# Kernel tuning notes

Measured on AMD Instinct MI355X. Metric: run time of the kernel, lower is better.

The kernel has to match this reference:

```python
import jax, jax.numpy as jnp
import numpy as np

H, DM, DX = 4, 64, 64  # num_heads, out_m_dim, out_x_dim
IN_L, IN_M, IN_X = 128, 128, 128
N, E, E2 = 10000, 160000, 320000


def _edge_softmax(scores, dst, num_nodes):
    # scores: [n_edges, H, 1]; softmax over edges sharing the same dst node
    mx = jax.ops.segment_max(scores, dst, num_segments=num_nodes)
    ex = jnp.exp(scores - mx[dst])
    denom = jax.ops.segment_sum(ex, dst, num_segments=num_nodes)
    return ex / denom[dst]


def setup_inputs() -> dict:
    key = jax.random.key(0)
    ks = jax.random.split(key, 24)

    def xn(k, shape):
        fan = sum(shape)
        return jax.random.normal(k, shape, dtype=jnp.float32) * np.sqrt(2.0 / fan)

    inp = {
        'l_feats': jax.random.normal(ks[0], (N, IN_L), dtype=jnp.float32),
        'm_feats': jax.random.normal(ks[1], (E, IN_M), dtype=jnp.float32),
        'x_feats': jax.random.normal(ks[2], (E2, IN_X), dtype=jnp.float32),
        'g_src': jax.random.randint(ks[3], (E,), 0, N, dtype=jnp.int32),
        'g_dst': jax.random.randint(ks[4], (E,), 0, N, dtype=jnp.int32),
        'lg_src': jax.random.randint(ks[5], (E2,), 0, E, dtype=jnp.int32),
        'lg_dst': jax.random.randint(ks[6], (E2,), 0, E, dtype=jnp.int32),
        # line-graph branch params (torch Linear convention: W [out, in])
        'W_lg_node': xn(ks[7], (DM * H, IN_M + IN_X)),
        'b_lg_node': jnp.zeros((DM * H,), dtype=jnp.float32),
        'W_lg_ni': xn(ks[8], (DX * H, IN_M)),
        'W_lg_fij': xn(ks[9], (DX * H, IN_X)),
        'W_lg_nj': xn(ks[10], (DX * H, IN_M)),
        'lg_attn': xn(ks[11], (1, H, DX)),
        'bias_lg': jnp.zeros((H * DX,), dtype=jnp.float32),
        # base-graph branch params
        'W_g_node': xn(ks[12], (DM * H, IN_M + IN_L)),
        'b_g_node': jnp.zeros((DM * H,), dtype=jnp.float32),
        'W_g_ni': xn(ks[13], (DM * H, IN_L)),
        'W_g_fij': xn(ks[14], (DM * H, IN_M)),
        'W_g_nj': xn(ks[15], (DM * H, IN_L)),
        'g_attn': xn(ks[16], (1, H, DM)),
        'bias_g': jnp.zeros((H * DM,), dtype=jnp.float32),
    }
    return inp


def reference(l_feats, m_feats, x_feats,
              W_lg_node, b_lg_node, W_lg_ni, W_lg_fij, W_lg_nj, lg_attn, bias_lg,
              W_g_node, b_g_node, W_g_ni, W_g_fij, W_g_nj, g_attn, bias_g,
              g_src, g_dst, lg_src, lg_dst):
    n_nodes = l_feats.shape[0]      # graph nodes
    n_lnodes = m_feats.shape[0]     # l_graph nodes == graph edges
    lrelu = jax.nn.leaky_relu       # slope 0.01 (torch default)

    # ---- line-graph attention branch ----
    lg_f_ni = m_feats @ W_lg_ni.T                      # [E, H*DX]
    lg_f_nj = m_feats @ W_lg_nj.T
    lg_f_fij = x_feats @ W_lg_fij.T                    # [E2, H*DX]
    lg_f_out = lrelu(lg_f_ni[lg_src] + lg_f_nj[lg_dst] + lg_f_fij + bias_lg)
    xr = lg_f_out.reshape(-1, H, DX)                   # [E2, H, DX]
    lg_e = jnp.sum(xr * lg_attn, axis=-1, keepdims=True)  # [E2, H, 1]
    a_lg = _edge_softmax(lg_e, lg_dst, n_lnodes)       # [E2, H, 1]

    # mean-aggregate l_graph edge feats onto dst nodes (DGL send_and_recv mean)
    cnt = jax.ops.segment_sum(jnp.ones((lg_dst.shape[0],), dtype=x_feats.dtype),
                              lg_dst, num_segments=n_lnodes)
    agg = jax.ops.segment_sum(x_feats, lg_dst, num_segments=n_lnodes)
    agg = agg / jnp.maximum(cnt, 1.0)[:, None]         # [E, IN_X]

    m1 = jnp.concatenate([m_feats, agg], axis=1)       # [E, IN_M+IN_X]
    h1 = (m1 @ W_lg_node.T + b_lg_node).reshape(-1, H, DM)
    msg1 = h1[lg_src] * a_lg                           # u_mul_e
    h1_dst = jax.ops.segment_sum(msg1, lg_dst, num_segments=n_lnodes)
    lg_h_out = jnp.sum(lrelu(h1_dst), axis=1)          # [E, DM]

    # ---- base-graph attention branch ----
    g_f_ni = l_feats @ W_g_ni.T                        # [N, H*DM]
    g_f_nj = l_feats @ W_g_nj.T
    g_f_fij = m_feats @ W_g_fij.T                      # [E, H*DM]
    g_f_out = lrelu(g_f_ni[g_src] + g_f_nj[g_dst] + g_f_fij + bias_g)
    g_f_out = g_f_out.reshape(-1, H, DM)               # [E, H, DM]
    g_e = jnp.sum(g_f_out * g_attn, axis=-1, keepdims=True)  # [E, H, 1]

    node_edge = l_feats[g_src] + l_feats[g_dst]        # [E, IN_L]
    m2 = jnp.concatenate([node_edge, m_feats], axis=1)  # [E, IN_L+IN_M]
    h2 = (m2 @ W_g_node.T + b_g_node).reshape(-1, H, DM)
    a_g = _edge_softmax(g_e, g_dst, n_nodes)           # [E, H, 1] (per graph edge)
    # l_graph.update_all(u_mul_v): msg[e2] = h2[src(e2)] * a_g[dst(e2)]
    msg2 = h2[lg_src] * a_g[lg_dst]
    h2_dst = jax.ops.segment_sum(msg2, lg_dst, num_segments=n_lnodes)
    g_h_out = jnp.sum(lrelu(h2_dst), axis=1)           # [E, DM]

    return g_h_out + lg_h_out                          # [E, DM]
```

## Files before the change

kernel.cpp:

```cpp
#include <hip/hip_runtime.h>
#include <math.h>

#define LRELU(x) ((x) > 0.0f ? (x) : 0.01f * (x))

typedef __attribute__((ext_vector_type(8))) short short8;
typedef __attribute__((ext_vector_type(4))) float f32x4;

__device__ __forceinline__ unsigned fenc(float f) {
    unsigned u = __float_as_uint(f);
    return (u & 0x80000000u) ? ~u : (u | 0x80000000u);
}
__device__ __forceinline__ float fdec(unsigned u) {
    return __uint_as_float((u & 0x80000000u) ? (u & 0x7FFFFFFFu) : ~u);
}
__device__ __forceinline__ unsigned short f2bf(float f) {
    unsigned u = __float_as_uint(f);
    u += 0x7FFFu + ((u >> 16) & 1u);
    return (unsigned short)(u >> 16);
}
__device__ __forceinline__ float bf2f(unsigned short b) {
    return __uint_as_float(((unsigned)b) << 16);
}
__device__ __forceinline__ ushort4 cvt4(float4 v) {
    ushort4 p;
    p.x = f2bf(v.x); p.y = f2bf(v.y); p.z = f2bf(v.z); p.w = f2bf(v.w);
    return p;
}

__global__ __launch_bounds__(256) void f2bf_k(
    const float* __restrict__ in, unsigned short* __restrict__ out, int n)
{
    for (int i = blockIdx.x * 256 + threadIdx.x; i < n; i += gridDim.x * 256)
        out[i] = f2bf(in[i]);
}

__global__ __launch_bounds__(256) void gemm128_mfma(
    const float* __restrict__ A, const unsigned short* __restrict__ Wbf,
    const float* __restrict__ biasf, unsigned short* __restrict__ Cout, int M)
{
    __shared__ __align__(16) unsigned short smem[64 * 264];
    const int row0 = blockIdx.x * 64;
    const int tid = threadIdx.x;
    const int wv = tid >> 6, lane = tid & 63;
    const int ln = lane & 15, quad = lane >> 4;

    float4 va[8];
#pragma unroll
    for (int k = 0; k < 8; ++k) {
        int i = tid + k * 256;
        int r = row0 + (i >> 5);
        va[k] = make_float4(0.f, 0.f, 0.f, 0.f);
        if (r < M) va[k] = *(const float4*)&A[(size_t)r * 128 + (i & 31) * 4];
    }
#pragma unroll
    for (int k = 0; k < 8; ++k) {
        int i = tid + k * 256;
        *(ushort4*)&smem[(i >> 5) * 136 + (i & 31) * 4] = cvt4(va[k]);
    }
    __syncthreads();

    f32x4 acc[16];
#pragma unroll
    for (int t = 0; t < 16; ++t) acc[t] = (f32x4){0.f, 0.f, 0.f, 0.f};

#pragma unroll 1
    for (int ks = 0; ks < 4; ++ks) {
        short8 a = *(const short8*)&smem[(wv * 16 + ln) * 136 + ks * 32 + quad * 8];
#pragma unroll
        for (int t = 0; t < 16; ++t) {
            short8 b = *(const short8*)&Wbf[(size_t)(t * 16 + ln) * 128 + ks * 32 + quad * 8];
            acc[t] = __builtin_amdgcn_mfma_f32_16x16x32_bf16(a, b, acc[t], 0, 0, 0);
        }
    }
    __syncthreads();

#pragma unroll
    for (int t = 0; t < 16; ++t) {
        int col = t * 16 + ln;
        float bb = biasf ? biasf[col] : 0.0f;
#pragma unroll
        for (int rg = 0; rg < 4; ++rg)
            smem[(wv * 16 + quad * 4 + rg) * 264 + col] = f2bf(acc[t][rg] + bb);
    }
    __syncthreads();
#pragma unroll 1
    for (int i = tid; i < 2048; i += 256) {
        int row = i >> 5, c8 = (i & 31) * 8;
        int r = row0 + row;
        if (r < M) *(short8*)&Cout[(size_t)r * 256 + c8] = *(const short8*)&smem[row * 264 + c8];
    }
}

__global__ __launch_bounds__(256) void gemm_score_mfma(
    const float* __restrict__ A, const unsigned short* __restrict__ Wbf,
    const unsigned short* __restrict__ fni, const unsigned short* __restrict__ fnj,
    const float* __restrict__ bias, const float* __restrict__ attn,
    const int* __restrict__ src, const int* __restrict__ dst,
    float* __restrict__ ebuf, unsigned* __restrict__ smax, int M, int domax)
{
    __shared__ __align__(16) unsigned short smem[64 * 264];
    const int row0 = blockIdx.x * 64;
    const int tid = threadIdx.x;
    const int wv = tid >> 6, lane = tid & 63;
    const int ln = lane & 15, quad = lane >> 4;

    const int rbase = row0 + wv * 16;
    int myr = rbase + ln;
    int msrc = 0, mdst = 0;
    if (myr < M) { msrc = src[myr]; mdst = dst[myr]; }

    float4 va[8];
#pragma unroll
    for (int k = 0; k < 8; ++k) {
        int i = tid + k * 256;
        int r = row0 + (i >> 5);
        va[k] = make_float4(0.f, 0.f, 0.f, 0.f);
        if (r < M) va[k] = *(const float4*)&A[(size_t)r * 128 + (i & 31) * 4];
    }
#pragma unroll
    for (int k = 0; k < 8; ++k) {
        int i = tid + k * 256;
        *(ushort4*)&smem[(i >> 5) * 136 + (i & 31) * 4] = cvt4(va[k]);
    }
    __syncthreads();

    f32x4 acc[16];
#pragma unroll
    for (int t = 0; t < 16; ++t) acc[t] = (f32x4){0.f, 0.f, 0.f, 0.f};

#pragma unroll 1
    for (int ks = 0; ks < 4; ++ks) {
        short8 a = *(const short8*)&smem[(wv * 16 + ln) * 136 + ks * 32 + quad * 8];
#pragma unroll
        for (int t = 0; t < 16; ++t) {
            short8 b = *(const short8*)&Wbf[(size_t)(t * 16 + ln) * 128 + ks * 32 + quad * 8];
            acc[t] = __builtin_amdgcn_mfma_f32_16x16x32_bf16(a, b, acc[t], 0, 0, 0);
        }
    }
    __syncthreads();

    const int c4 = lane * 4;
    const float4 bias4 = *(const float4*)&bias[c4];
    const float4 attn4 = *(const float4*)&attn[c4];

    ushort4 pu[16], pv[16];
#pragma unroll
    for (int j = 0; j < 16; ++j) {
        int s_ = __shfl(msrc, j, 16);
        int d_ = __shfl(mdst, j, 16);
        pu[j] = *(const ushort4*)&fni[(size_t)s_ * 256 + c4];
        pv[j] = *(const ushort4*)&fnj[(size_t)d_ * 256 + c4];
    }

#pragma unroll
    for (int t = 0; t < 16; ++t) {
        int col = t * 16 + ln;
#pragma unroll
        for (int rg = 0; rg < 4; ++rg)
            smem[(wv * 16 + quad * 4 + rg) * 264 + col] = f2bf(acc[t][rg]);
    }

#pragma unroll
    for (int i = 0; i < 16; ++i) {
        int rr = wv * 16 + i;
        int r = row0 + rr;
        if (r >= M) continue;
        int dIdx = __shfl(mdst, i, 16);
        ushort4 f4 = *(const ushort4*)&smem[rr * 264 + c4];
        float v0 = bf2f(f4.x) + bf2f(pu[i].x) + bf2f(pv[i].x) + bias4.x;
        float v1 = bf2f(f4.y) + bf2f(pu[i].y) + bf2f(pv[i].y) + bias4.y;
        float v2 = bf2f(f4.z) + bf2f(pu[i].z) + bf2f(pv[i].z) + bias4.z;
        float v3 = bf2f(f4.w) + bf2f(pu[i].w) + bf2f(pv[i].w) + bias4.w;
        float p = LRELU(v0) * attn4.x + LRELU(v1) * attn4.y
                + LRELU(v2) * attn4.z + LRELU(v3) * attn4.w;
        p += __shfl_xor(p, 1, 64);
        p += __shfl_xor(p, 2, 64);
        p += __shfl_xor(p, 4, 64);
        p += __shfl_xor(p, 8, 64);
        if (ln == 0) {
            ebuf[(size_t)r * 4 + quad] = p;
            if (domax) atomicMax(&smax[(size_t)dIdx * 4 + quad], fenc(p));
        }
    }
}

__global__ __launch_bounds__(256) void gemm256_mfma(
    const float* __restrict__ A0, const void* __restrict__ A1v,
    const int* __restrict__ gsrc, const int* __restrict__ gdst,
    const unsigned short* __restrict__ Wbf, const float* __restrict__ biasf,
    unsigned short* __restrict__ Cout, int M, int mode)
{
    __shared__ __align__(16) unsigned short smem[64 * 264];
    const int row0 = blockIdx.x * 64;
    const int tid = threadIdx.x;
    const int wv = tid >> 6, lane = tid & 63;
    const int ln = lane & 15, quad = lane >> 4;

    if (mode == 0) {
        const unsigned short* A1 = (const unsigned short*)A1v;
        float4 va[8];
#pragma unroll
        for (int k = 0; k < 8; ++k) {
            int i = tid + k * 256;
            int r = row0 + (i >> 5);
            va[k] = make_float4(0.f, 0.f, 0.f, 0.f);
            if (r < M) va[k] = *(const float4*)&A0[(size_t)r * 128 + (i & 31) * 4];
        }
        short8 vb[4];
#pragma unroll
        for (int k = 0; k < 4; ++k) {
            int i = tid + k * 256;
            int r = row0 + (i >> 4);
#pragma unroll
            for (int q = 0; q < 8; ++q) vb[k][q] = 0;
            if (r < M) vb[k] = *(const short8*)&A1[(size_t)r * 128 + (i & 15) * 8];
        }
#pragma unroll
        for (int k = 0; k < 8; ++k) {
            int i = tid + k * 256;
            *(ushort4*)&smem[(i >> 5) * 264 + (i & 31) * 4] = cvt4(va[k]);
        }
#pragma unroll
        for (int k = 0; k < 4; ++k) {
            int i = tid + k * 256;
            *(short8*)&smem[(i >> 4) * 264 + 128 + (i & 15) * 8] = vb[k];
        }
    } else {
        const float* A1 = (const float*)A1v;
        int is[8], id[8];
#pragma unroll
        for (int k = 0; k < 8; ++k) {
            int i = tid + k * 256;
            int r = row0 + (i >> 5);
            is[k] = (r < M) ? gsrc[r] : 0;
            id[k] = (r < M) ? gdst[r] : 0;
        }
        float4 va[8], vb2[8], vc[8];
#pragma unroll
        for (int k = 0; k < 8; ++k) {
            int i = tid + k * 256;
            int r = row0 + (i >> 5);
            int c4i = (i & 31) * 4;
            va[k]  = *(const float4*)&A0[(size_t)is[k] * 128 + c4i];
            vb2[k] = *(const float4*)&A0[(size_t)id[k] * 128 + c4i];
            vc[k] = make_float4(0.f, 0.f, 0.f, 0.f);
            if (r < M) vc[k] = *(const float4*)&A1[(size_t)r * 128 + c4i];
        }
#pragma unroll
        for (int k = 0; k < 8; ++k) {
            int i = tid + k * 256;
            int r = row0 + (i >> 5);
            int c4i = (i & 31) * 4;
            float4 v = make_float4(va[k].x + vb2[k].x, va[k].y + vb2[k].y,
                                   va[k].z + vb2[k].z, va[k].w + vb2[k].w);
            if (r >= M) v = make_float4(0.f, 0.f, 0.f, 0.f);
            *(ushort4*)&smem[(i >> 5) * 264 + c4i] = cvt4(v);
            *(ushort4*)&smem[(i >> 5) * 264 + 128 + c4i] = cvt4(vc[k]);
        }
    }
    __syncthreads();

    f32x4 acc[16];
#pragma unroll
    for (int t = 0; t < 16; ++t) acc[t] = (f32x4){0.f, 0.f, 0.f, 0.f};

#pragma unroll 1
    for (int ks = 0; ks < 8; ++ks) {
        short8 a = *(const short8*)&smem[(wv * 16 + ln) * 264 + ks * 32 + quad * 8];
#pragma unroll
        for (int t = 0; t < 16; ++t) {
            short8 b = *(const short8*)&Wbf[(size_t)(t * 16 + ln) * 256 + ks * 32 + quad * 8];
            acc[t] = __builtin_amdgcn_mfma_f32_16x16x32_bf16(a, b, acc[t], 0, 0, 0);
        }
    }
    __syncthreads();

#pragma unroll
    for (int t = 0; t < 16; ++t) {
        int col = t * 16 + ln;
        float bb = biasf[col];
#pragma unroll
        for (int rg = 0; rg < 4; ++rg)
            smem[(wv * 16 + quad * 4 + rg) * 264 + col] = f2bf(acc[t][rg] + bb);
    }
    __syncthreads();
#pragma unroll 1
    for (int i = tid; i < 2048; i += 256) {
        int row = i >> 5, c8 = (i & 31) * 8;
        int r = row0 + row;
        if (r < M) *(short8*)&Cout[(size_t)r * 256 + c8] = *(const short8*)&smem[row * 264 + c8];
    }
}

__global__ __launch_bounds__(256) void edge_exp(
    float* __restrict__ ebuf, const unsigned* __restrict__ smax,
    float* __restrict__ sden, const int* __restrict__ dst, int nE)
{
    int i = blockIdx.x * 256 + threadIdx.x;
    if (i >= nE * 4) return;
    int e = i >> 2, h = i & 3;
    int d = dst[e];
    float m = fdec(smax[(size_t)d * 4 + h]);
    float ex = expf(ebuf[i] - m);
    ebuf[i] = ex;
    atomicAdd(&sden[(size_t)d * 4 + h], ex);
}

__global__ __launch_bounds__(256) void count_k(
    const int* __restrict__ dst, int* __restrict__ cnt, int n)
{
    int i = blockIdx.x * 256 + threadIdx.x;
    if (i < n) atomicAdd(&cnt[dst[i]], 1);
}

__global__ __launch_bounds__(256) void scan1(
    const int* __restrict__ cnt, int* __restrict__ excl, int* __restrict__ bsum, int n)
{
    __shared__ int sd[256];
    int tid = threadIdx.x;
    int i = blockIdx.x * 256 + tid;
    int v = (i < n) ? cnt[i] : 0;
    sd[tid] = v;
    __syncthreads();
    for (int off2 = 1; off2 < 256; off2 <<= 1) {
        int t = (tid >= off2) ? sd[tid - off2] : 0;
        __syncthreads();
        sd[tid] += t;
        __syncthreads();
    }
    if (i < n) excl[i] = sd[tid] - v;
    if (tid == 255) bsum[blockIdx.x] = sd[255];
}

__global__ __launch_bounds__(1024) void scan2(int* __restrict__ bsum, int nb)
{
    __shared__ int sd[1024];
    int tid = threadIdx.x;
    int v = (tid < nb) ? bsum[tid] : 0;
    sd[tid] = v;
    __syncthreads();
    for (int off2 = 1; off2 < 1024; off2 <<= 1) {
        int t = (tid >= off2) ? sd[tid - off2] : 0;
        __syncthreads();
        sd[tid] += t;
        __syncthreads();
    }
    if (tid < nb) bsum[tid] = sd[tid] - v;
}

__global__ __launch_bounds__(256) void scan3(
    int* __restrict__ excl, const int* __restrict__ bsum, int n, int total)
{
    int i = blockIdx.x * 256 + threadIdx.x;
    if (i < n) excl[i] += bsum[i >> 8];
    if (i == 0) excl[n] = total;
}

__global__ __launch_bounds__(256) void fill_k(
    const int* __restrict__ dst, const int* __restrict__ row_ptr,
    int* __restrict__ cursor, int* __restrict__ colidx, int n)
{
    int i = blockIdx.x * 256 + threadIdx.x;
    if (i >= n) return;
    int d = dst[i];
    int p = atomicAdd(&cursor[d], 1);
    colidx[row_ptr[d] + p] = i;
}

__global__ __launch_bounds__(256) void agg_gather(
    const int* __restrict__ row_ptr, const int* __restrict__ colidx,
    const float* __restrict__ x, unsigned short* __restrict__ aggbf, int nE)
{
    const int lane = threadIdx.x & 63;
    const int d = blockIdx.x * 4 + (threadIdx.x >> 6);
    if (d >= nE) return;
    int b = row_ptr[d], en = row_ptr[d + 1];
    float s0 = 0.f, s1 = 0.f;
    for (int k = b; k < en; ++k) {
        int e = colidx[k];
        float2 v = *(const float2*)&x[(size_t)e * 128 + lane * 2];
        s0 += v.x; s1 += v.y;
    }
    float c = fmaxf((float)(en - b), 1.0f);
    ushort2 o;
    o.x = f2bf(s0 / c); o.y = f2bf(s1 / c);
    *(ushort2*)&aggbf[(size_t)d * 128 + lane * 2] = o;
}

__global__ __launch_bounds__(256) void final_agg(
    const int* __restrict__ row_ptr, const int* __restrict__ colidx,
    const int* __restrict__ lg_src, const float* __restrict__ e_lg,
    const unsigned* __restrict__ lgmax,
    const unsigned short* __restrict__ h1, const unsigned short* __restrict__ h2,
    const float* __restrict__ e_g, const float* __restrict__ gden,
    const int* __restrict__ g_dst, float* __restrict__ out, int nE)
{
    const int lane = threadIdx.x & 63;
    const int d = blockIdx.x * 4 + (threadIdx.x >> 6);
    if (d >= nE) return;
    int b = row_ptr[d], en = row_ptr[d + 1];

    uint4 mu = *(const uint4*)&lgmax[(size_t)d * 4];
    float mx0 = fdec(mu.x), mx1 = fdec(mu.y), mx2 = fdec(mu.z), mx3 = fdec(mu.w);

    float den0 = 0.f, den1 = 0.f, den2 = 0.f, den3 = 0.f;
    float a10 = 0.f, a11 = 0.f, a12 = 0.f, a13 = 0.f;
    float a20 = 0.f, a21 = 0.f, a22 = 0.f, a23 = 0.f;
    for (int k = b; k < en; ++k) {
        int e = colidx[k];
        float4 sc = *(const float4*)&e_lg[(size_t)e * 4];
        float w0 = expf(sc.x - mx0), w1 = expf(sc.y - mx1);
        float w2 = expf(sc.z - mx2), w3 = expf(sc.w - mx3);
        den0 += w0; den1 += w1; den2 += w2; den3 += w3;
        int s = lg_src[e];
        const unsigned short* p1 = &h1[(size_t)s * 256 + lane];
        const unsigned short* p2 = &h2[(size_t)s * 256 + lane];
        a10 += bf2f(p1[0])   * w0;
        a11 += bf2f(p1[64])  * w1;
        a12 += bf2f(p1[128]) * w2;
        a13 += bf2f(p1[192]) * w3;
        a20 += bf2f(p2[0]);
        a21 += bf2f(p2[64]);
        a22 += bf2f(p2[128]);
        a23 += bf2f(p2[192]);
    }
    float o = 0.f;
    if (en > b) {
        float v0 = a10 / den0, v1 = a11 / den1, v2 = a12 / den2, v3 = a13 / den3;
        o += LRELU(v0) + LRELU(v1) + LRELU(v2) + LRELU(v3);
    }
    int gd = g_dst[d];
    float g0 = e_g[(size_t)d * 4 + 0] / gden[(size_t)gd * 4 + 0] * a20;
    float g1 = e_g[(size_t)d * 4 + 1] / gden[(size_t)gd * 4 + 1] * a21;
    float g2 = e_g[(size_t)d * 4 + 2] / gden[(size_t)gd * 4 + 2] * a22;
    float g3 = e_g[(size_t)d * 4 + 3] / gden[(size_t)gd * 4 + 3] * a23;
    o += LRELU(g0) + LRELU(g1) + LRELU(g2) + LRELU(g3);
    out[(size_t)d * 64 + lane] = o;
}

extern "C" void kernel_launch(void* const* d_in, const int* in_sizes, int n_in,
                              void* d_out, int out_size, void* d_ws, size_t ws_size,
                              hipStream_t stream)
{
    const float* l_feats   = (const float*)d_in[0];
    const float* m_feats   = (const float*)d_in[1];
    const float* x_feats   = (const float*)d_in[2];
    const int*   g_src     = (const int*)d_in[3];
    const int*   g_dst     = (const int*)d_in[4];
    const int*   lg_src    = (const int*)d_in[5];
    const int*   lg_dst    = (const int*)d_in[6];
    const float* W_lg_node = (const float*)d_in[7];
    const float* b_lg_node = (const float*)d_in[8];
    const float* W_lg_ni   = (const float*)d_in[9];
    const float* W_lg_fij  = (const float*)d_in[10];
    const float* W_lg_nj   = (const float*)d_in[11];
    const float* lg_attn   = (const float*)d_in[12];
    const float* bias_lg   = (const float*)d_in[13];
    const float* W_g_node  = (const float*)d_in[14];
    const float* b_g_node  = (const float*)d_in[15];
    const float* W_g_ni    = (const float*)d_in[16];
    const float* W_g_fij   = (const float*)d_in[17];
    const float* W_g_nj    = (const float*)d_in[18];
    const float* g_attn    = (const float*)d_in[19];
    const float* bias_g    = (const float*)d_in[20];

    const int N  = in_sizes[0] / 128;
    const int E  = in_sizes[3];
    const int E2 = in_sizes[5];

    float* ws = (float*)d_ws;
    size_t off = 0;
    auto alloc = [&](size_t n) { float* p = ws + off; off += n; return p; };

    unsigned short* wbuf = (unsigned short*)alloc(163840);
    unsigned short* wgni_bf    = wbuf;
    unsigned short* wgnj_bf    = wbuf + 32768;
    unsigned short* wlgni_bf   = wbuf + 65536;
    unsigned short* wlgnj_bf   = wbuf + 98304;
    unsigned short* wlgfij_bf  = wbuf + 131072;
    unsigned short* wgfij_bf   = wbuf + 163840;
    unsigned short* wlgnode_bf = wbuf + 196608;
    unsigned short* wgnode_bf  = wbuf + 262144;

    unsigned short* ni_lg = (unsigned short*)alloc((size_t)E * 128);
    unsigned short* nj_lg = (unsigned short*)alloc((size_t)E * 128);
    unsigned short* gni   = (unsigned short*)alloc((size_t)N * 128);
    unsigned short* gnj   = (unsigned short*)alloc((size_t)N * 128);
    unsigned short* aggbf = (unsigned short*)alloc((size_t)E * 64);
    float* e_lg  = alloc((size_t)E2 * 4);
    float* e_g   = alloc((size_t)E * 4);
    unsigned* gmax = (unsigned*)alloc((size_t)N * 4);
    float* gden  = alloc((size_t)N * 4);
    unsigned* lgmax = (unsigned*)alloc((size_t)E * 4);
    int* row_ptr = (int*)alloc((size_t)E + 4);
    int* colidx  = (int*)alloc((size_t)E2);
    int* cnt     = (int*)alloc((size_t)E);
    int* cursor  = (int*)alloc((size_t)E);
    int* bsum    = (int*)alloc(1024);

    unsigned short* h1 = ni_lg;
    unsigned short* h2 = nj_lg;

    (void)n_in; (void)out_size; (void)ws_size;
    float* outp = (float*)d_out;
    dim3 blk(256);

    hipMemsetAsync(cnt,    0, (size_t)E * 4, stream);
    hipMemsetAsync(cursor, 0, (size_t)E * 4, stream);
    hipMemsetAsync(gmax,   0, (size_t)N * 4 * 4, stream);
    hipMemsetAsync(gden,   0, (size_t)N * 4 * 4, stream);
    hipMemsetAsync(lgmax,  0, (size_t)E * 4 * 4, stream);

    f2bf_k<<<128, blk, 0, stream>>>(W_g_ni,    wgni_bf,    32768);
    f2bf_k<<<128, blk, 0, stream>>>(W_g_nj,    wgnj_bf,    32768);
    f2bf_k<<<128, blk, 0, stream>>>(W_lg_ni,   wlgni_bf,   32768);
    f2bf_k<<<128, blk, 0, stream>>>(W_lg_nj,   wlgnj_bf,   32768);
    f2bf_k<<<128, blk, 0, stream>>>(W_lg_fij,  wlgfij_bf,  32768);
    f2bf_k<<<128, blk, 0, stream>>>(W_g_fij,   wgfij_bf,   32768);
    f2bf_k<<<256, blk, 0, stream>>>(W_lg_node, wlgnode_bf, 65536);
    f2bf_k<<<256, blk, 0, stream>>>(W_g_node,  wgnode_bf,  65536);

    const int nb = (E + 255) / 256;
    count_k<<<(E2 + 255) / 256, blk, 0, stream>>>(lg_dst, cnt, E2);
    scan1<<<nb, blk, 0, stream>>>(cnt, row_ptr, bsum, E);
    scan2<<<1, 1024, 0, stream>>>(bsum, nb);
    scan3<<<nb, blk, 0, stream>>>(row_ptr, bsum, E, E2);
    fill_k<<<(E2 + 255) / 256, blk, 0, stream>>>(lg_dst, row_ptr, cursor, colidx, E2);

    gemm128_mfma<<<(N + 63) / 64, blk, 0, stream>>>(l_feats, wgni_bf, nullptr, gni, N);
    gemm128_mfma<<<(N + 63) / 64, blk, 0, stream>>>(l_feats, wgnj_bf, nullptr, gnj, N);
    gemm128_mfma<<<(E + 63) / 64, blk, 0, stream>>>(m_feats, wlgni_bf, nullptr, ni_lg, E);
    gemm128_mfma<<<(E + 63) / 64, blk, 0, stream>>>(m_feats, wlgnj_bf, nullptr, nj_lg, E);

    gemm_score_mfma<<<(E2 + 63) / 64, blk, 0, stream>>>(
        x_feats, wlgfij_bf, ni_lg, nj_lg, bias_lg, lg_attn, lg_src, lg_dst,
        e_lg, lgmax, E2, 1);
    gemm_score_mfma<<<(E + 63) / 64, blk, 0, stream>>>(
        m_feats, wgfij_bf, gni, gnj, bias_g, g_attn, g_src, g_dst,
        e_g, gmax, E, 1);

    edge_exp<<<(unsigned)(((long long)E * 4 + 255) / 256), blk, 0, stream>>>(e_g, gmax, gden, g_dst, E);

    agg_gather<<<(E + 3) / 4, blk, 0, stream>>>(row_ptr, colidx, x_feats, aggbf, E);

    gemm256_mfma<<<(E + 63) / 64, blk, 0, stream>>>(
        m_feats, (const void*)aggbf, nullptr, nullptr, wlgnode_bf, b_lg_node, h1, E, 0);
    gemm256_mfma<<<(E + 63) / 64, blk, 0, stream>>>(
        l_feats, (const void*)m_feats, g_src, g_dst, wgnode_bf, b_g_node, h2, E, 1);

    final_agg<<<(E + 3) / 4, blk, 0, stream>>>(
        row_ptr, colidx, lg_src, e_lg, lgmax, h1, h2, e_g, gden, g_dst, outp, E);
}
```

Before: 1.446 ms.

## Load MFMA A-fragments directly from global, fuse dual GEMMs, pre-convert m_feats to bf16

Drops the LDS staging of the A operand in the GEMM kernels: each lane now loads its MFMA A fragment straight from global memory, which removes the block-wide __syncthreads and lets each wave write out its own rows. The ni/nj projection pairs are merged into one dual kernel per input, so A is read once and both outputs are produced. m_feats is converted to bf16 once and reused by four GEMMs, and the eight weight-conversion launches become a single kernel. In exchange, the per-lane global A loads are less coalesced, the kernels use more registers, and an extra bf16 copy of m_feats is written if workspace allows.

Result: slower. 1.567 ms (+8.4%).

```diff
diff --git a/kernel.cpp b/kernel.cpp
--- a/kernel.cpp
+++ b/kernel.cpp
@@ -27,117 +27,156 @@
     return p;
 }
 
-__global__ __launch_bounds__(256) void f2bf_k(
-    const float* __restrict__ in, unsigned short* __restrict__ out, int n)
-{
-    for (int i = blockIdx.x * 256 + threadIdx.x; i < n; i += gridDim.x * 256)
-        out[i] = f2bf(in[i]);
-}
-
-__global__ __launch_bounds__(256) void gemm128_mfma(
-    const float* __restrict__ A, const unsigned short* __restrict__ Wbf,
-    const float* __restrict__ biasf, unsigned short* __restrict__ Cout, int M)
+__device__ __forceinline__ void load_frag4(
+    const void* __restrict__ Av, int is_bf16, size_t row, int quad, short8* a)
+{
+    if (is_bf16) {
+        const unsigned short* A = (const unsigned short*)Av;
+#pragma unroll
+        for (int ks = 0; ks < 4; ++ks)
+            a[ks] = *(const short8*)&A[row * 128 + ks * 32 + quad * 8];
+    } else {
+        const float* A = (const float*)Av;
+#pragma unroll
+        for (int ks = 0; ks < 4; ++ks) {
+            int cc = ks * 32 + quad * 8;
+            float4 u0 = *(const float4*)&A[row * 128 + cc];
+            float4 u1 = *(const float4*)&A[row * 128 + cc + 4];
+            ushort4 lo = cvt4(u0), hi = cvt4(u1);
+            a[ks][0] = lo.x; a[ks][1] = lo.y; a[ks][2] = lo.z; a[ks][3] = lo.w;
+            a[ks][4] = hi.x; a[ks][5] = hi.y; a[ks][6] = hi.z; a[ks][7] = hi.w;
+        }
+    }
+}
+
+__global__ __launch_bounds__(256) void wcvt_k(
+    const float* __restrict__ s0, const float* __restrict__ s1,
+    const float* __restrict__ s2, const float* __restrict__ s3,
+    const float* __restrict__ s4, const float* __restrict__ s5,
+    const float* __restrict__ s6, const float* __restrict__ s7,
+    unsigned short* __restrict__ dst)
+{
+    long long e = ((long long)blockIdx.x * 256 + threadIdx.x) * 4;
+    if (e >= 327680) return;
+    int c = (int)(e >> 15);
+    const float* s;
+    long long off = e & 32767;
+    switch (c) {
+        case 0: s = s0; break;
+        case 1: s = s1; break;
+        case 2: s = s2; break;
+        case 3: s = s3; break;
+        case 4: s = s4; break;
+        case 5: s = s5; break;
+        case 6: s = s6; break;
+        case 7: s = s6; off += 32768; break;
+        case 8: s = s7; break;
+        default: s = s7; off += 32768; break;
+    }
+    float4 v = *(const float4*)&s[off];
+    *(ushort4*)&dst[e] = cvt4(v);
+}
+
+__global__ __launch_bounds__(256) void cvt1_k(
+    const float* __restrict__ in, unsigned short* __restrict__ out, int n4)
+{
+    int stride = gridDim.x * 256;
+    for (int u = blockIdx.x * 256 + threadIdx.x; u < n4; u += stride) {
+        float4 v = *(const float4*)&in[(size_t)u * 4];
+        *(ushort4*)&out[(size_t)u * 4] = cvt4(v);
+    }
+}
+
+__global__ __launch_bounds__(256) void gemm128_dual(
+    const void* __restrict__ Av, int a_is_bf16,
+    const unsigned short* __restrict__ Wbf,
+    unsigned short* __restrict__ C1, unsigned short* __restrict__ C2, int M)
 {
     __shared__ __align__(16) unsigned short smem[64 * 264];
-    const int row0 = blockIdx.x * 64;
     const int tid = threadIdx.x;
     const int wv = tid >> 6, lane = tid & 63;
     const int ln = lane & 15, quad = lane >> 4;
-
-    float4 va[8];
-#pragma unroll
-    for (int k = 0; k < 8; ++k) {
-        int i = tid + k * 256;
-        int r = row0 + (i >> 5);
-        va[k] = make_float4(0.f, 0.f, 0.f, 0.f);
-        if (r < M) va[k] = *(const float4*)&A[(size_t)r * 128 + (i & 31) * 4];
-    }
-#pragma unroll
-    for (int k = 0; k < 8; ++k) {
-        int i = tid + k * 256;
-        *(ushort4*)&smem[(i >> 5) * 136 + (i & 31) * 4] = cvt4(va[k]);
-    }
-    __syncthreads();
-
-    f32x4 acc[16];
-#pragma unroll
-    for (int t = 0; t < 16; ++t) acc[t] = (f32x4){0.f, 0.f, 0.f, 0.f};
+    const int row0 = blockIdx.x * 64;
+    const int myr = row0 + wv * 16 + ln;
+
+    short8 a[4];
+#pragma unroll
+    for (int ks = 0; ks < 4; ++ks)
+#pragma unroll
+        for (int q = 0; q < 8; ++q) a[ks][q] = 0;
+    if (myr < M) load_frag4(Av, a_is_bf16, (size_t)myr, quad, a);
 
 #pragma unroll 1
-    for (int ks = 0; ks < 4; ++ks) {
-        short8 a = *(const short8*)&smem[(wv * 16 + ln) * 136 + ks * 32 + quad * 8];
+    for (int h = 0; h < 2; ++h) {
+        f32x4 acc[16];
+#pragma unroll
+        for (int t = 0; t < 16; ++t) acc[t] = (f32x4){0.f, 0.f, 0.f, 0.f};
+        const unsigned short* W = Wbf + (size_t)h * 256 * 128;
+#pragma unroll
+        for (int ks = 0; ks < 4; ++ks) {
+#pragma unroll
+            for (int t = 0; t < 16; ++t) {
+                short8 b = *(const short8*)&W[(size_t)(t * 16 + ln) * 128 + ks * 32 + quad * 8];
+                acc[t] = __builtin_amdgcn_mfma_f32_16x16x32_bf16(a[ks], b, acc[t], 0, 0, 0);
+            }
+        }
 #pragma unroll
         for (int t = 0; t < 16; ++t) {
-            short8 b = *(const short8*)&Wbf[(size_t)(t * 16 + ln) * 128 + ks * 32 + quad * 8];
-            acc[t] = __builtin_amdgcn_mfma_f32_16x16x32_bf16(a, b, acc[t], 0, 0, 0);
-        }
-    }
-    __syncthreads();
-
-#pragma unroll
-    for (int t = 0; t < 16; ++t) {
-        int col = t * 16 + ln;
-        float bb = biasf ? biasf[col] : 0.0f;
-#pragma unroll
-        for (int rg = 0; rg < 4; ++rg)
-            smem[(wv * 16 + quad * 4 + rg) * 264 + col] = f2bf(acc[t][rg] + bb);
-    }
-    __syncthreads();
-#pragma unroll 1
-    for (int i = tid; i < 2048; i += 256) {
-        int row = i >> 5, c8 = (i & 31) * 8;
-        int r = row0 + row;
-        if (r < M) *(short8*)&Cout[(size_t)r * 256 + c8] = *(const short8*)&smem[row * 264 + c8];
+            int col = t * 16 + ln;
+#pragma unroll
+            for (int rg = 0; rg < 4; ++rg)
+                smem[(wv * 16 + quad * 4 + rg) * 264 + col] = f2bf(acc[t][rg]);
+        }
+        asm volatile("" ::: "memory");
+        unsigned short* C = h ? C2 : C1;
+#pragma unroll
+        for (int k = 0; k < 8; ++k) {
+            int j = lane + k * 64;
+            int row = j >> 5, c8 = (j & 31) * 8;
+            int r = row0 + wv * 16 + row;
+            if (r < M)
+                *(short8*)&C[(size_t)r * 256 + c8] = *(const short8*)&smem[(wv * 16 + row) * 264 + c8];
+        }
+        asm volatile("" ::: "memory");
     }
 }
 
 __global__ __launch_bounds__(256) void gemm_score_mfma(
-    const float* __restrict__ A, const unsigned short* __restrict__ Wbf,
+    const void* __restrict__ Av, int a_is_bf16,
+    const unsigned short* __restrict__ Wbf,
     const unsigned short* __restrict__ fni, const unsigned short* __restrict__ fnj,
     const float* __restrict__ bias, const float* __restrict__ attn,
     const int* __restrict__ src, const int* __restrict__ dst,
-    float* __restrict__ ebuf, unsigned* __restrict__ smax, int M, int domax)
+    float* __restrict__ ebuf, unsigned* __restrict__ smax, int M)
 {
     __shared__ __align__(16) unsigned short smem[64 * 264];
-    const int row0 = blockIdx.x * 64;
     const int tid = threadIdx.x;
     const int wv = tid >> 6, lane = tid & 63;
     const int ln = lane & 15, quad = lane >> 4;
-
-    const int rbase = row0 + wv * 16;
-    int myr = rbase + ln;
+    const int row0 = blockIdx.x * 64;
+    const int myr = row0 + wv * 16 + ln;
+
     int msrc = 0, mdst = 0;
     if (myr < M) { msrc = src[myr]; mdst = dst[myr]; }
 
-    float4 va[8];
-#pragma unroll
-    for (int k = 0; k < 8; ++k) {
-        int i = tid + k * 256;
-        int r = row0 + (i >> 5);
-        va[k] = make_float4(0.f, 0.f, 0.f, 0.f);
-        if (r < M) va[k] = *(const float4*)&A[(size_t)r * 128 + (i & 31) * 4];
-    }
-#pragma unroll
-    for (int k = 0; k < 8; ++k) {
-        int i = tid + k * 256;
-        *(ushort4*)&smem[(i >> 5) * 136 + (i & 31) * 4] = cvt4(va[k]);
-    }
-    __syncthreads();
+    short8 a[4];
+#pragma unroll
+    for (int ks = 0; ks < 4; ++ks)
+#pragma unroll
+        for (int q = 0; q < 8; ++q) a[ks][q] = 0;
+    if (myr < M) load_frag4(Av, a_is_bf16, (size_t)myr, quad, a);
 
     f32x4 acc[16];
 #pragma unroll
     for (int t = 0; t < 16; ++t) acc[t] = (f32x4){0.f, 0.f, 0.f, 0.f};
-
-#pragma unroll 1
+#pragma unroll
     for (int ks = 0; ks < 4; ++ks) {
-        short8 a = *(const short8*)&smem[(wv * 16 + ln) * 136 + ks * 32 + quad * 8];
 #pragma unroll
         for (int t = 0; t < 16; ++t) {
             short8 b = *(const short8*)&Wbf[(size_t)(t * 16 + ln) * 128 + ks * 32 + quad * 8];
-            acc[t] = __builtin_amdgcn_mfma_f32_16x16x32_bf16(a, b, acc[t], 0, 0, 0);
-        }
-    }
-    __syncthreads();
+            acc[t] = __builtin_amdgcn_mfma_f32_16x16x32_bf16(a[ks], b, acc[t], 0, 0, 0);
+        }
+    }
 
     const int c4 = lane * 4;
     const float4 bias4 = *(const float4*)&bias[c4];
@@ -159,6 +198,7 @@
         for (int rg = 0; rg < 4; ++rg)
             smem[(wv * 16 + quad * 4 + rg) * 264 + col] = f2bf(acc[t][rg]);
     }
+    asm volatile("" ::: "memory");
 
 #pragma unroll
     for (int i = 0; i < 16; ++i) {
@@ -179,101 +219,64 @@
         p += __shfl_xor(p, 8, 64);
         if (ln == 0) {
             ebuf[(size_t)r * 4 + quad] = p;
-            if (domax) atomicMax(&smax[(size_t)dIdx * 4 + quad], fenc(p));
+            atomicMax(&smax[(size_t)dIdx * 4 + quad], fenc(p));
         }
     }
 }
 
 __global__ __launch_bounds__(256) void gemm256_mfma(
-    const float* __restrict__ A0, const void* __restrict__ A1v,
+    const void* __restrict__ Mv, int m_is_bf16,
+    const unsigned short* __restrict__ Aux, const float* __restrict__ lf,
     const int* __restrict__ gsrc, const int* __restrict__ gdst,
     const unsigned short* __restrict__ Wbf, const float* __restrict__ biasf,
     unsigned short* __restrict__ Cout, int M, int mode)
 {
     __shared__ __align__(16) unsigned short smem[64 * 264];
-    const int row0 = blockIdx.x * 64;
     const int tid = threadIdx.x;
     const int wv = tid >> 6, lane = tid & 63;
     const int ln = lane & 15, quad = lane >> 4;
-
-    if (mode == 0) {
-        const unsigned short* A1 = (const unsigned short*)A1v;
-        float4 va[8];
-#pragma unroll
-        for (int k = 0; k < 8; ++k) {
-            int i = tid + k * 256;
-            int r = row0 + (i >> 5);
-            va[k] = make_float4(0.f, 0.f, 0.f, 0.f);
-            if (r < M) va[k] = *(const float4*)&A0[(size_t)r * 128 + (i & 31) * 4];
-        }
-        short8 vb[4];
-#pragma unroll
-        for (int k = 0; k < 4; ++k) {
-            int i = tid + k * 256;
-            int r = row0 + (i >> 4);
-#pragma unroll
-            for (int q = 0; q < 8; ++q) vb[k][q] = 0;
-            if (r < M) vb[k] = *(const short8*)&A1[(size_t)r * 128 + (i & 15) * 8];
-        }
-#pragma unroll
-        for (int k = 0; k < 8; ++k) {
-            int i = tid + k * 256;
-            *(ushort4*)&smem[(i >> 5) * 264 + (i & 31) * 4] = cvt4(va[k]);
-        }
-#pragma unroll
-        for (int k = 0; k < 4; ++k) {
-            int i = tid + k * 256;
-            *(short8*)&smem[(i >> 4) * 264 + 128 + (i & 15) * 8] = vb[k];
-        }
-    } else {
-        const float* A1 = (const float*)A1v;
-        int is[8], id[8];
-#pragma unroll
-        for (int k = 0; k < 8; ++k) {
-            int i = tid + k * 256;
-            int r = row0 + (i >> 5);
-            is[k] = (r < M) ? gsrc[r] : 0;
-            id[k] = (r < M) ? gdst[r] : 0;
-        }
-        float4 va[8], vb2[8], vc[8];
-#pragma unroll
-        for (int k = 0; k < 8; ++k) {
-            int i = tid + k * 256;
-            int r = row0 + (i >> 5);
-            int c4i = (i & 31) * 4;
-            va[k]  = *(const float4*)&A0[(size_t)is[k] * 128 + c4i];
-            vb2[k] = *(const float4*)&A0[(size_t)id[k] * 128 + c4i];
-            vc[k] = make_float4(0.f, 0.f, 0.f, 0.f);
-            if (r < M) vc[k] = *(const float4*)&A1[(size_t)r * 128 + c4i];
-        }
-#pragma unroll
-        for (int k = 0; k < 8; ++k) {
-            int i = tid + k * 256;
-            int r = row0 + (i >> 5);
-            int c4i = (i & 31) * 4;
-            float4 v = make_float4(va[k].x + vb2[k].x, va[k].y + vb2[k].y,
-                                   va[k].z + vb2[k].z, va[k].w + vb2[k].w);
-            if (r >= M) v = make_float4(0.f, 0.f, 0.f, 0.f);
-            *(ushort4*)&smem[(i >> 5) * 264 + c4i] = cvt4(v);
-            *(ushort4*)&smem[(i >> 5) * 264 + 128 + c4i] = cvt4(vc[k]);
-        }
-    }
-    __syncthreads();
+    const int row0 = blockIdx.x * 64;
+    const int myr = row0 + wv * 16 + ln;
+
+    short8 a[8];
+#pragma unroll
+    for (int ks = 0; ks < 8; ++ks)
+#pragma unroll
+        for (int q = 0; q < 8; ++q) a[ks][q] = 0;
+
+    if (myr < M) {
+        if (mode == 0) {
+            load_frag4(Mv, m_is_bf16, (size_t)myr, quad, a);
+            load_frag4(Aux, 1, (size_t)myr, quad, a + 4);
+        } else {
+            int s = gsrc[myr], d = gdst[myr];
+#pragma unroll
+            for (int ks = 0; ks < 4; ++ks) {
+                int cc = ks * 32 + quad * 8;
+                float4 u0 = *(const float4*)&lf[(size_t)s * 128 + cc];
+                float4 u1 = *(const float4*)&lf[(size_t)s * 128 + cc + 4];
+                float4 w0 = *(const float4*)&lf[(size_t)d * 128 + cc];
+                float4 w1 = *(const float4*)&lf[(size_t)d * 128 + cc + 4];
+                ushort4 lo = cvt4(make_float4(u0.x + w0.x, u0.y + w0.y, u0.z + w0.z, u0.w + w0.w));
+                ushort4 hi = cvt4(make_float4(u1.x + w1.x, u1.y + w1.y, u1.z + w1.z, u1.w + w1.w));
+                a[ks][0] = lo.x; a[ks][1] = lo.y; a[ks][2] = lo.z; a[ks][3] = lo.w;
+                a[ks][4] = hi.x; a[ks][5] = hi.y; a[ks][6] = hi.z; a[ks][7] = hi.w;
+            }
+            load_frag4(Mv, m_is_bf16, (size_t)myr, quad, a + 4);
+        }
+    }
 
     f32x4 acc[16];
 #pragma unroll
     for (int t = 0; t < 16; ++t) acc[t] = (f32x4){0.f, 0.f, 0.f, 0.f};
-
-#pragma unroll 1
+#pragma unroll
     for (int ks = 0; ks < 8; ++ks) {
-        short8 a = *(const short8*)&smem[(wv * 16 + ln) * 264 + ks * 32 + quad * 8];
 #pragma unroll
         for (int t = 0; t < 16; ++t) {
             short8 b = *(const short8*)&Wbf[(size_t)(t * 16 + ln) * 256 + ks * 32 + quad * 8];
-            acc[t] = __builtin_amdgcn_mfma_f32_16x16x32_bf16(a, b, acc[t], 0, 0, 0);
-        }
-    }
-    __syncthreads();
+            acc[t] = __builtin_amdgcn_mfma_f32_16x16x32_bf16(a[ks], b, acc[t], 0, 0, 0);
+        }
+    }
 
 #pragma unroll
     for (int t = 0; t < 16; ++t) {
@@ -283,12 +286,14 @@
         for (int rg = 0; rg < 4; ++rg)
             smem[(wv * 16 + quad * 4 + rg) * 264 + col] = f2bf(acc[t][rg] + bb);
     }
-    __syncthreads();
-#pragma unroll 1
-    for (int i = tid; i < 2048; i += 256) {
-        int row = i >> 5, c8 = (i & 31) * 8;
-        int r = row0 + row;
-        if (r < M) *(short8*)&Cout[(size_t)r * 256 + c8] = *(const short8*)&smem[row * 264 + c8];
+    asm volatile("" ::: "memory");
+#pragma unroll
+    for (int k = 0; k < 8; ++k) {
+        int j = lane + k * 64;
+        int row = j >> 5, c8 = (j & 31) * 8;
+        int r = row0 + wv * 16 + row;
+        if (r < M)
+            *(short8*)&Cout[(size_t)r * 256 + c8] = *(const short8*)&smem[(wv * 16 + row) * 264 + c8];
     }
 }
 
@@ -473,10 +478,8 @@
     auto alloc = [&](size_t n) { float* p = ws + off; off += n; return p; };
 
     unsigned short* wbuf = (unsigned short*)alloc(163840);
-    unsigned short* wgni_bf    = wbuf;
-    unsigned short* wgnj_bf    = wbuf + 32768;
-    unsigned short* wlgni_bf   = wbuf + 65536;
-    unsigned short* wlgnj_bf   = wbuf + 98304;
+    unsigned short* wgni_pair  = wbuf;
+    unsigned short* wlgni_pair = wbuf + 65536;
     unsigned short* wlgfij_bf  = wbuf + 131072;
     unsigned short* wgfij_bf   = wbuf + 163840;
     unsigned short* wlgnode_bf = wbuf + 196608;
@@ -498,10 +501,14 @@
     int* cursor  = (int*)alloc((size_t)E);
     int* bsum    = (int*)alloc(1024);
 
+    const int use_mbf = ((off + (size_t)E * 64) * sizeof(float) <= ws_size) ? 1 : 0;
+    unsigned short* mbf = use_mbf ? (unsigned short*)alloc((size_t)E * 64) : nullptr;
+    const void* mA = use_mbf ? (const void*)mbf : (const void*)m_feats;
+
     unsigned short* h1 = ni_lg;
     unsigned short* h2 = nj_lg;
 
-    (void)n_in; (void)out_size; (void)ws_size;
+    (void)n_in; (void)out_size;
     float* outp = (float*)d_out;
     dim3 blk(256);
 
@@ -511,14 +518,10 @@
     hipMemsetAsync(gden,   0, (size_t)N * 4 * 4, stream);
     hipMemsetAsync(lgmax,  0, (size_t)E * 4 * 4, stream);
 
-    f2bf_k<<<128, blk, 0, stream>>>(W_g_ni,    wgni_bf,    32768);
-    f2bf_k<<<128, blk, 0, stream>>>(W_g_nj,    wgnj_bf,    32768);
-    f2bf_k<<<128, blk, 0, stream>>>(W_lg_ni,   wlgni_bf,   32768);
-    f2bf_k<<<128, blk, 0, stream>>>(W_lg_nj,   wlgnj_bf,   32768);
-    f2bf_k<<<128, blk, 0, stream>>>(W_lg_fij,  wlgfij_bf,  32768);
-    f2bf_k<<<128, blk, 0, stream>>>(W_g_fij,   wgfij_bf,   32768);
-    f2bf_k<<<256, blk, 0, stream>>>(W_lg_node, wlgnode_bf, 65536);
-    f2bf_k<<<256, blk, 0, stream>>>(W_g_node,  wgnode_bf,  65536);
+    wcvt_k<<<320, blk, 0, stream>>>(W_g_ni, W_g_nj, W_lg_ni, W_lg_nj,
+                                    W_lg_fij, W_g_fij, W_lg_node, W_g_node, wbuf);
+    if (use_mbf)
+        cvt1_k<<<2048, blk, 0, stream>>>(m_feats, mbf, E * 32);
 
     const int nb = (E + 255) / 256;
     count_k<<<(E2 + 255) / 256, blk, 0, stream>>>(lg_dst, cnt, E2);
@@ -527,26 +530,24 @@
     scan3<<<nb, blk, 0, stream>>>(row_ptr, bsum, E, E2);
     fill_k<<<(E2 + 255) / 256, blk, 0, stream>>>(lg_dst, row_ptr, cursor, colidx, E2);
 
-    gemm128_mfma<<<(N + 63) / 64, blk, 0, stream>>>(l_feats, wgni_bf, nullptr, gni, N);
-    gemm128_mfma<<<(N + 63) / 64, blk, 0, stream>>>(l_feats, wgnj_bf, nullptr, gnj, N);
-    gemm128_mfma<<<(E + 63) / 64, blk, 0, stream>>>(m_feats, wlgni_bf, nullptr, ni_lg, E);
-    gemm128_mfma<<<(E + 63) / 64, blk, 0, stream>>>(m_feats, wlgnj_bf, nullptr, nj_lg, E);
+    gemm128_dual<<<(N + 63) / 64, blk, 0, stream>>>(l_feats, 0, wgni_pair, gni, gnj, N);
+    gemm128_dual<<<(E + 63) / 64, blk, 0, stream>>>(mA, use_mbf, wlgni_pair, ni_lg, nj_lg, E);
 
     gemm_score_mfma<<<(E2 + 63) / 64, blk, 0, stream>>>(
-        x_feats, wlgfij_bf, ni_lg, nj_lg, bias_lg, lg_attn, lg_src, lg_dst,
-        e_lg, lgmax, E2, 1);
+        x_feats, 0, wlgfij_bf, ni_lg, nj_lg, bias_lg, lg_attn, lg_src, lg_dst,
+        e_lg, lgmax, E2);
     gemm_score_mfma<<<(E + 63) / 64, blk, 0, stream>>>(
-        m_feats, wgfij_bf, gni, gnj, bias_g, g_attn, g_src, g_dst,
-        e_g, gmax, E, 1);
+        mA, use_mbf, wgfij_bf, gni, gnj, bias_g, g_attn, g_src, g_dst,
+        e_g, gmax, E);
 
     edge_exp<<<(unsigned)(((long long)E * 4 + 255) / 256), blk, 0, stream>>>(e_g, gmax, gden, g_dst, E);
 
     agg_gather<<<(E + 3) / 4, blk, 0, stream>>>(row_ptr, colidx, x_feats, aggbf, E);
 
     gemm256_mfma<<<(E + 63) / 64, blk, 0, stream>>>(
-        m_feats, (const void*)aggbf, nullptr, nullptr, wlgnode_bf, b_lg_node, h1, E, 0);
+        mA, use_mbf, aggbf, nullptr, nullptr, nullptr, wlgnode_bf, b_lg_node, h1, E, 0);
     gemm256_mfma<<<(E + 63) / 64, blk, 0, stream>>>(
-        l_feats, (const void*)m_feats, g_src, g_dst, wgnode_bf, b_g_node, h2, E, 1);
+        mA, use_mbf, nullptr, l_feats, g_src, g_dst, wgnode_bf, b_g_node, h2, E, 1);
 
     final_agg<<<(E + 3) / 4, blk, 0, stream>>>(
         row_ptr, colidx, lg_src, e_lg, lgmax, h1, h2, e_g, gden, g_dst, outp, E);
```
